# Kernel tuning notes

Measured on AMD Instinct MI355X. Metric: run time of the kernel, lower is better.

The kernel has to match this reference:

```python
import jax, jax.numpy as jnp
import numpy as np

S = 8192      # total patch tokens
NSEG = 8      # number of images/segments (equal length)
D = 1280      # embed dim
H = 16        # heads
HD = 80       # head dim
MLP = 3456    # swiglu hidden


def setup_inputs() -> dict:
    key = jax.random.key(0)
    ks = jax.random.split(key, 8)
    def w(k, shape):
        return jax.random.normal(k, shape, jnp.float32) * 0.02
    return {
        "x": jax.random.normal(ks[0], (S, 1, D), jnp.float32),
        "rotary_pos_emb": jax.random.uniform(ks[1], (S, HD // 2), jnp.float32) * 6.2831853,
        "cu_seqlens": jnp.arange(NSEG + 1, dtype=jnp.int32) * (S // NSEG),
        "norm1_w": jnp.ones((D,), jnp.float32), "norm1_b": jnp.zeros((D,), jnp.float32),
        "norm2_w": jnp.ones((D,), jnp.float32), "norm2_b": jnp.zeros((D,), jnp.float32),
        "w_qkv": w(ks[2], (3 * D, D)), "b_qkv": jnp.zeros((3 * D,), jnp.float32),
        "w_proj": w(ks[3], (D, D)), "b_proj": jnp.zeros((D,), jnp.float32),
        "w_gate": w(ks[4], (MLP, D)), "b_gate": jnp.zeros((MLP,), jnp.float32),
        "w_up": w(ks[5], (MLP, D)), "b_up": jnp.zeros((MLP,), jnp.float32),
        "w_down": w(ks[6], (D, MLP)), "b_down": jnp.zeros((D,), jnp.float32),
    }


def _ln(x, w, b, eps=1e-6):
    m = x.mean(-1, keepdims=True)
    v = ((x - m) ** 2).mean(-1, keepdims=True)
    return (x - m) * jax.lax.rsqrt(v + eps) * w + b


def _rope(x, cos, sin):
    # x: [B, S, H, HD]; cos/sin: [S, HD/2]; non-interleaved (chunk-halves) rotation
    c = jnp.concatenate([cos, cos], -1)[None, :, None, :]
    s = jnp.concatenate([sin, sin], -1)[None, :, None, :]
    x1, x2 = jnp.split(x, 2, -1)
    return x * c + jnp.concatenate([-x2, x1], -1) * s


def _forward(cu, x, freqs, norm1_w, norm1_b, norm2_w, norm2_b,
             w_qkv, b_qkv, w_proj, b_proj,
             w_gate, b_gate, w_up, b_up, w_down, b_down):
    S_, B, D_ = x.shape  # B == 1
    L = int(cu[1] - cu[0])          # equal-length segments
    nseg = len(cu) - 1
    h = _ln(x, norm1_w, norm1_b)
    qkv = h @ w_qkv.T + b_qkv                                   # [S, B, 3D]
    q, k, v = jnp.split(qkv, 3, -1)
    q, k, v = (t.reshape(S_, B, H, HD).transpose(1, 0, 2, 3) for t in (q, k, v))  # [B,S,H,d]
    cos, sin = jnp.cos(freqs), jnp.sin(freqs)
    q = _rope(q, cos, sin)
    k = _rope(k, cos, sin)
    # block-diagonal attention over cu_seqlens: fold segments into batch
    qs, ks_, vs = (t.reshape(B * nseg, L, H, HD) for t in (q, k, v))
    scale = 1.0 / np.float32(np.sqrt(HD))
    scores = jnp.einsum('blhd,bmhd->bhlm', qs, ks_) * scale     # [nseg,H,L,L]
    attn = jax.nn.softmax(scores, axis=-1)
    ctx = jnp.einsum('bhlm,bmhd->blhd', attn, vs)               # [nseg,L,H,d]
    ctx = ctx.reshape(B, S_, H * HD).transpose(1, 0, 2)         # [S,B,D]
    x = x + ctx @ w_proj.T + b_proj
    h2 = _ln(x, norm2_w, norm2_b)
    gate = jax.nn.silu(h2 @ w_gate.T + b_gate)
    up = h2 @ w_up.T + b_up
    return x + (gate * up) @ w_down.T + b_down


def reference(x, rotary_pos_emb, cu_seqlens, norm1_w, norm1_b, norm2_w, norm2_b,
              w_qkv, b_qkv, w_proj, b_proj, w_gate, b_gate, w_up, b_up,
              w_down, b_down):
    cu = np.asarray(cu_seqlens)
    return _forward(cu, x, rotary_pos_emb, norm1_w, norm1_b, norm2_w, norm2_b,
                    w_qkv, b_qkv, w_proj, b_proj,
                    w_gate, b_gate, w_up, b_up, w_down, b_down)
```

## Files before the change

### kernel.cpp

```cpp
#include <hip/hip_runtime.h>


#define S_TOK 8192
#define DIM   1280
#define NHEAD 16
#define HDIM  80
#define SEGLEN 1024
#define MLPD  3456

typedef __attribute__((ext_vector_type(8))) short bf16x8;
typedef __attribute__((ext_vector_type(8))) unsigned short u16x8;
typedef __attribute__((ext_vector_type(4))) float f32x4;

__device__ __forceinline__ float bf2f(unsigned short u) {
    unsigned int x = ((unsigned int)u) << 16;
    return __builtin_bit_cast(float, x);
}
__device__ __forceinline__ unsigned short f2bf(float f) {
    unsigned int x = __builtin_bit_cast(unsigned int, f);
    unsigned int r = x + 0x7fffu + ((x >> 16) & 1u);
    return (unsigned short)(r >> 16);
}

__device__ __forceinline__ void gload_lds16(const void* g, void* l) {
    __builtin_amdgcn_global_load_lds(
        (const __attribute__((address_space(1))) void*)g,
        (__attribute__((address_space(3))) void*)l, 16, 0, 0);
}

__device__ __forceinline__ int xcd_swz(int bid, int nwg) {
    const int q = nwg >> 3, r = nwg & 7;
    const int x = bid & 7, j = bid >> 3;
    return (x < r ? x * (q + 1) : r * (q + 1) + (x - r) * q) + j;
}

__global__ __launch_bounds__(256)
void f2b_kernel(const float* __restrict__ in, unsigned short* __restrict__ out, int n4)
{
    const int i = blockIdx.x * 256 + threadIdx.x;
    if (i >= n4) return;
    const float4 v = ((const float4*)in)[i];
    ushort4 o;
    o.x = f2bf(v.x); o.y = f2bf(v.y); o.z = f2bf(v.z); o.w = f2bf(v.w);
    ((ushort4*)out)[i] = o;
}

__global__ __launch_bounds__(256)
void ln_kernel(const float* __restrict__ xin,
               const float* __restrict__ w,
               const float* __restrict__ b,
               unsigned short* __restrict__ out)
{
    const int row = blockIdx.x;
    const int t = threadIdx.x;
    const size_t base = (size_t)row * DIM;
    float v[5];
#pragma unroll
    for (int i = 0; i < 5; ++i) v[i] = xin[base + t + i * 256];
    float s = 0.f, s2 = 0.f;
#pragma unroll
    for (int i = 0; i < 5; ++i) { s += v[i]; s2 += v[i] * v[i]; }
#pragma unroll
    for (int off = 32; off > 0; off >>= 1) {
        s  += __shfl_down(s, off);
        s2 += __shfl_down(s2, off);
    }
    __shared__ float rs[8];
    const int wave = t >> 6, lane = t & 63;
    if (lane == 0) { rs[wave] = s; rs[wave + 4] = s2; }
    __syncthreads();
    s  = rs[0] + rs[1] + rs[2] + rs[3];
    s2 = rs[4] + rs[5] + rs[6] + rs[7];
    const float mean = s * (1.f / DIM);
    const float var  = s2 * (1.f / DIM) - mean * mean;
    const float rstd = rsqrtf(var + 1e-6f);
#pragma unroll
    for (int i = 0; i < 5; ++i) {
        const int c = t + i * 256;
        out[base + c] = f2bf((v[i] - mean) * rstd * w[c] + b[c]);
    }
}

__global__ __launch_bounds__(256)
void rope_kernel(const unsigned short* __restrict__ qkv,
                 const float* __restrict__ rot,
                 unsigned short* __restrict__ qr,
                 unsigned short* __restrict__ kr)
{
    const int idx = blockIdx.x * 256 + threadIdx.x;
    const int s = idx / DIM, rem = idx % DIM;
    const int h = rem / HDIM, d = rem % HDIM;
    const int dd = (d < 40) ? d : d - 40;
    const float th = rot[s * 40 + dd];
    const float c = __cosf(th), sn = __sinf(th);
    const size_t base = (size_t)s * (3 * DIM) + h * HDIM;
    const int partner = (d < 40) ? d + 40 : d - 40;
    const float sgn = (d < 40) ? -1.f : 1.f;
    const float q  = bf2f(qkv[base + d]);
    const float k  = bf2f(qkv[DIM + base + d]);
    const float qp = bf2f(qkv[base + partner]);
    const float kp = bf2f(qkv[DIM + base + partner]);
    const float qo = q * c + sgn * qp * sn;
    const float ko = k * c + sgn * kp * sn;
    qr[idx] = f2bf(qo * 0.11180339887498949f);
    kr[idx] = f2bf(ko);
}

enum { EPI_BF16 = 0, EPI_RES = 1, EPI_GU = 2 };

template<int EPI>
__global__ __launch_bounds__(512, 2)
void gemm4q(const unsigned short* __restrict__ A,
            const unsigned short* __restrict__ B0,
            const unsigned short* __restrict__ B1,
            const float* __restrict__ bias0,
            const float* __restrict__ bias1,
            void* __restrict__ C,
            const void* __restrict__ aux,
            int M, int N, int K, int ntn)
{
    extern __shared__ __align__(16) unsigned short lds[];
    const int t = threadIdx.x;
    const int w = t >> 6, lane = t & 63;
    const int m = lane & 15, g = lane >> 4;
    const int wm = w >> 2, wn = w & 3;
    const int wg = xcd_swz(blockIdx.x, gridDim.x);
    const int nblk = wg % ntn;
    const int m0 = (wg / ntn) * 256;
    const int NT = K >> 6;

    f32x4 acc[8][4] = {};

    auto STAGE_A = [&](int tt) {
        const int k0 = tt << 6;
        unsigned short* dst = lds + (tt & 1) * 16384;
#pragma unroll
        for (int i = 0; i < 4; ++i) {
            const int ch = i * 512 + t;
            const int row = ch >> 3, c = ch & 7;
            gload_lds16(A + (size_t)(m0 + row) * K + k0 + (c ^ (row & 7)) * 8,
                        dst + ch * 8);
        }
    };
    auto STAGE_B = [&](int tt) {
        const int k0 = tt << 6;
        unsigned short* dst = lds + 32768 + (tt & 1) * 16384;
#pragma unroll
        for (int i = 0; i < 4; ++i) {
            const int ch = i * 512 + t;
            const int row = ch >> 3, c = ch & 7;
            const unsigned short* src;
            if (EPI == EPI_GU) {
                src = (row < 128)
                    ? B0 + (size_t)(nblk * 128 + row) * K
                    : B1 + (size_t)(nblk * 128 + (row - 128)) * K;
            } else {
                src = B0 + (size_t)(nblk * 256 + row) * K;
            }
            gload_lds16(src + k0 + (c ^ (row & 7)) * 8, dst + ch * 8);
        }
    };

    STAGE_A(0); STAGE_B(0);
    asm volatile("s_waitcnt vmcnt(0)" ::: "memory");
    __builtin_amdgcn_s_barrier();

    for (int tt = 0; tt < NT; ++tt) {
        const unsigned short* As = lds + (tt & 1) * 16384;
        const unsigned short* Bs = lds + 32768 + (tt & 1) * 16384;
        bf16x8 bfr[4];
#pragma unroll
        for (int kk = 0; kk < 2; ++kk) {
#pragma unroll
            for (int mh = 0; mh < 2; ++mh) {
                bf16x8 afr[4];
                const int cs = ((kk * 4 + g) ^ (m & 7)) * 8;
#pragma unroll
                for (int mf4 = 0; mf4 < 4; ++mf4) {
                    const int row = wm * 128 + (mh * 4 + mf4) * 16 + m;
                    afr[mf4] = *(const bf16x8*)&As[row * 64 + cs];
                }
                if (mh == 0) {
#pragma unroll
                    for (int nf = 0; nf < 4; ++nf) {
                        int rowb;
                        if (EPI == EPI_GU)
                            rowb = (nf < 2) ? (wn * 32 + nf * 16 + m)
                                            : (128 + wn * 32 + (nf - 2) * 16 + m);
                        else
                            rowb = wn * 64 + nf * 16 + m;
                        bfr[nf] = *(const bf16x8*)&Bs[rowb * 64 + cs];
                    }
                }
                if (kk == 0 && mh == 0 && tt + 1 < NT) STAGE_A(tt + 1);
                if (kk == 0 && mh == 1 && tt + 1 < NT) STAGE_B(tt + 1);
                if (kk == 1 && mh == 1)
                    asm volatile("s_waitcnt vmcnt(0)" ::: "memory");
                __builtin_amdgcn_s_barrier();
                __builtin_amdgcn_s_setprio(1);
#pragma unroll
                for (int mf4 = 0; mf4 < 4; ++mf4)
#pragma unroll
                    for (int nf = 0; nf < 4; ++nf)
                        acc[mh * 4 + mf4][nf] = __builtin_amdgcn_mfma_f32_16x16x32_bf16(
                            afr[mf4], bfr[nf], acc[mh * 4 + mf4][nf], 0, 0, 0);
                __builtin_amdgcn_s_setprio(0);
                __builtin_amdgcn_s_barrier();
            }
        }
    }

#pragma unroll
    for (int mf = 0; mf < 8; ++mf) {
        const int row = m0 + wm * 128 + mf * 16 + g * 4;
        if (EPI == EPI_GU) {
#pragma unroll
            for (int nfp = 0; nfp < 2; ++nfp) {
                const int col = nblk * 128 + wn * 32 + nfp * 16 + m;
                const float bgv = bias0[col], buv = bias1[col];
#pragma unroll
                for (int i = 0; i < 4; ++i) {
                    const float gv = acc[mf][nfp][i] + bgv;
                    const float uv = acc[mf][nfp + 2][i] + buv;
                    const float sg = gv / (1.f + __expf(-gv));
                    ((unsigned short*)C)[(size_t)(row + i) * N + col] = f2bf(sg * uv);
                }
            }
        } else {
#pragma unroll
            for (int nf = 0; nf < 4; ++nf) {
                const int col = nblk * 256 + wn * 64 + nf * 16 + m;
                const float bv = bias0[col];
#pragma unroll
                for (int i = 0; i < 4; ++i) {
                    const float v = acc[mf][nf][i] + bv;
                    const size_t idx = (size_t)(row + i) * N + col;
                    if (EPI == EPI_BF16) {
                        ((unsigned short*)C)[idx] = f2bf(v);
                    } else {
                        const float xr = ((const float*)aux)[idx];
                        ((float*)C)[idx] = v + xr;
                    }
                }
            }
        }
    }
}

__global__ __launch_bounds__(256)
void attn_mfma_kernel(const unsigned short* __restrict__ qr,
                      const unsigned short* __restrict__ kr,
                      const unsigned short* __restrict__ qkv,
                      unsigned short* __restrict__ ctx)
{
    const int qt = blockIdx.x, hh = blockIdx.y, seg = blockIdx.z;
    const int t = threadIdx.x;
    const int w = t >> 6, lane = t & 63;
    const int m = lane & 15, g = lane >> 4;

    __shared__ __align__(16) unsigned short Ks[64 * 80];
    __shared__ __align__(16) unsigned short Vt[80 * 72];
    __shared__ __align__(16) unsigned short Ps[4][16 * 72];

    const int q0 = seg * SEGLEN + qt * 64 + w * 16;

    bf16x8 qa0, qa1, qa2 = {};
    {
        const unsigned short* qrow = qr + (size_t)(q0 + m) * DIM + hh * HDIM;
        qa0 = *(const bf16x8*)(qrow + 8 * g);
        qa1 = *(const bf16x8*)(qrow + 32 + 8 * g);
        if (g < 2) qa2 = *(const bf16x8*)(qrow + 64 + 8 * g);
    }

    f32x4 o[5] = {};
    float mrow[4], lrow[4];
#pragma unroll
    for (int i = 0; i < 4; ++i) { mrow[i] = -1e30f; lrow[i] = 0.f; }

    for (int kt = 0; kt < SEGLEN / 64; ++kt) {
        const int kbase = seg * SEGLEN + kt * 64;
#pragma unroll
        for (int i = 0; i < 2; ++i) {
            const int ch = t + 256 * i;
            const int row = ch / 10, c = ch % 10;
            gload_lds16(kr + (size_t)(kbase + row) * DIM + hh * HDIM + c * 8,
                        &Ks[ch * 8]);
        }
        if (t < 128) {
            const int ch = 512 + t;
            const int row = ch / 10, c = ch % 10;
            gload_lds16(kr + (size_t)(kbase + row) * DIM + hh * HDIM + c * 8,
                        &Ks[ch * 8]);
        }
#pragma unroll
        for (int i = 0; i < 3; ++i) {
            const int ch = t + 256 * i;
            if (ch < 640) {
                const int k = ch & 63, dc = ch >> 6;
                const u16x8 v = *(const u16x8*)(qkv +
                    (size_t)(kbase + k) * (3 * DIM) + 2 * DIM + hh * HDIM + dc * 8);
#pragma unroll
                for (int e = 0; e < 8; ++e)
                    Vt[(dc * 8 + e) * 72 + k] = v[e];
            }
        }
        __syncthreads();

        f32x4 s[4] = {};
#pragma unroll
        for (int nn = 0; nn < 4; ++nn) {
            const unsigned short* kb = &Ks[(16 * nn + m) * 80];
            const bf16x8 b0 = *(const bf16x8*)(kb + 8 * g);
            const bf16x8 b1 = *(const bf16x8*)(kb + 32 + 8 * g);
            bf16x8 b2 = {};
            if (g < 2) b2 = *(const bf16x8*)(kb + 64 + 8 * g);
            s[nn] = __builtin_amdgcn_mfma_f32_16x16x32_bf16(qa0, b0, s[nn], 0, 0, 0);
            s[nn] = __builtin_amdgcn_mfma_f32_16x16x32_bf16(qa1, b1, s[nn], 0, 0, 0);
            s[nn] = __builtin_amdgcn_mfma_f32_16x16x32_bf16(qa2, b2, s[nn], 0, 0, 0);
        }

#pragma unroll
        for (int i = 0; i < 4; ++i) {
            float mx = fmaxf(fmaxf(s[0][i], s[1][i]), fmaxf(s[2][i], s[3][i]));
            mx = fmaxf(mx, __shfl_xor(mx, 1));
            mx = fmaxf(mx, __shfl_xor(mx, 2));
            mx = fmaxf(mx, __shfl_xor(mx, 4));
            mx = fmaxf(mx, __shfl_xor(mx, 8));
            const float mn = fmaxf(mrow[i], mx);
            const float fs = __expf(mrow[i] - mn);
            float rs = 0.f;
#pragma unroll
            for (int nn = 0; nn < 4; ++nn) {
                const float p = __expf(s[nn][i] - mn);
                s[nn][i] = p;
                rs += p;
            }
            rs += __shfl_xor(rs, 1);
            rs += __shfl_xor(rs, 2);
            rs += __shfl_xor(rs, 4);
            rs += __shfl_xor(rs, 8);
            lrow[i] = lrow[i] * fs + rs;
            mrow[i] = mn;
#pragma unroll
            for (int df = 0; df < 5; ++df) o[df][i] *= fs;
        }

#pragma unroll
        for (int nn = 0; nn < 4; ++nn)
#pragma unroll
            for (int i = 0; i < 4; ++i)
                Ps[w][(4 * g + i) * 72 + 16 * nn + m] = f2bf(s[nn][i]);

        const bf16x8 pa0 = *(const bf16x8*)&Ps[w][m * 72 + 8 * g];
        const bf16x8 pa1 = *(const bf16x8*)&Ps[w][m * 72 + 32 + 8 * g];
#pragma unroll
        for (int df = 0; df < 5; ++df) {
            const unsigned short* vb = &Vt[(16 * df + m) * 72];
            const bf16x8 vb0 = *(const bf16x8*)(vb + 8 * g);
            const bf16x8 vb1 = *(const bf16x8*)(vb + 32 + 8 * g);
            o[df] = __builtin_amdgcn_mfma_f32_16x16x32_bf16(pa0, vb0, o[df], 0, 0, 0);
            o[df] = __builtin_amdgcn_mfma_f32_16x16x32_bf16(pa1, vb1, o[df], 0, 0, 0);
        }
        __syncthreads();
    }

#pragma unroll
    for (int i = 0; i < 4; ++i) {
        const float inv = 1.f / lrow[i];
        unsigned short* crow = ctx + (size_t)(q0 + 4 * g + i) * DIM + hh * HDIM;
#pragma unroll
        for (int df = 0; df < 5; ++df)
            crow[16 * df + m] = f2bf(o[df][i] * inv);
    }
}

extern "C" void kernel_launch(void* const* d_in, const int* in_sizes, int n_in,
                              void* d_out, int out_size, void* d_ws, size_t ws_size,
                              hipStream_t stream)
{
    const float* x      = (const float*)d_in[0];
    const float* rot    = (const float*)d_in[1];
    const float* n1w    = (const float*)d_in[3];
    const float* n1b    = (const float*)d_in[4];
    const float* n2w    = (const float*)d_in[5];
    const float* n2b    = (const float*)d_in[6];
    const float* w_qkv  = (const float*)d_in[7];
    const float* b_qkv  = (const float*)d_in[8];
    const float* w_proj = (const float*)d_in[9];
    const float* b_proj = (const float*)d_in[10];
    const float* w_gate = (const float*)d_in[11];
    const float* b_gate = (const float*)d_in[12];
    const float* w_up   = (const float*)d_in[13];
    const float* b_up   = (const float*)d_in[14];
    const float* w_down = (const float*)d_in[15];
    const float* b_down = (const float*)d_in[16];

    char* ws = (char*)d_ws;
    unsigned short* qkv  = (unsigned short*)(ws + 0);
    unsigned short* h    = (unsigned short*)(ws + 62914560ull);
    unsigned short* qr   = (unsigned short*)(ws + 83886080ull);
    unsigned short* kr   = (unsigned short*)(ws + 104857600ull);
    unsigned short* ctx  = (unsigned short*)(ws + 125829120ull);
    float*          x2   = (float*)(ws + 146800640ull);
    unsigned short* wqb  = (unsigned short*)(ws + 188743680ull);
    unsigned short* wpb  = (unsigned short*)(ws + 198574080ull);
    unsigned short* wgb  = (unsigned short*)(ws + 201850880ull);
    unsigned short* wub  = (unsigned short*)(ws + 210698240ull);
    unsigned short* wdb  = (unsigned short*)(ws + 219545600ull);
    unsigned short* gbuf = qkv;

    hipFuncSetAttribute(reinterpret_cast<const void*>(gemm4q<EPI_BF16>),
                        hipFuncAttributeMaxDynamicSharedMemorySize, 131072);
    hipFuncSetAttribute(reinterpret_cast<const void*>(gemm4q<EPI_RES>),
                        hipFuncAttributeMaxDynamicSharedMemorySize, 131072);
    hipFuncSetAttribute(reinterpret_cast<const void*>(gemm4q<EPI_GU>),
                        hipFuncAttributeMaxDynamicSharedMemorySize, 131072);

    {
        const int nq = 3 * DIM * DIM / 4, np = DIM * DIM / 4, nm = MLPD * DIM / 4;
        f2b_kernel<<<(nq + 255) / 256, 256, 0, stream>>>(w_qkv,  wqb, nq);
        f2b_kernel<<<(np + 255) / 256, 256, 0, stream>>>(w_proj, wpb, np);
        f2b_kernel<<<(nm + 255) / 256, 256, 0, stream>>>(w_gate, wgb, nm);
        f2b_kernel<<<(nm + 255) / 256, 256, 0, stream>>>(w_up,   wub, nm);
        f2b_kernel<<<(nm + 255) / 256, 256, 0, stream>>>(w_down, wdb, nm);
    }

    ln_kernel<<<S_TOK, 256, 0, stream>>>(x, n1w, n1b, h);
    gemm4q<EPI_BF16><<<15 * 32, 512, 131072, stream>>>(
        h, wqb, nullptr, b_qkv, nullptr, qkv, nullptr, S_TOK, 3 * DIM, DIM, 15);
    rope_kernel<<<(S_TOK * DIM) / 256, 256, 0, stream>>>(qkv, rot, qr, kr);
    attn_mfma_kernel<<<dim3(SEGLEN / 64, NHEAD, S_TOK / SEGLEN), 256, 0, stream>>>(
        qr, kr, qkv, ctx);
    gemm4q<EPI_RES><<<5 * 32, 512, 131072, stream>>>(
        ctx, wpb, nullptr, b_proj, nullptr, x2, x, S_TOK, DIM, DIM, 5);
    ln_kernel<<<S_TOK, 256, 0, stream>>>(x2, n2w, n2b, h);
    gemm4q<EPI_GU><<<27 * 32, 512, 131072, stream>>>(
        h, wgb, wub, b_gate, b_up, gbuf, nullptr, S_TOK, MLPD, DIM, 27);
    gemm4q<EPI_RES><<<5 * 32, 512, 131072, stream>>>(
        gbuf, wdb, nullptr, b_down, nullptr, (float*)d_out, x2, S_TOK, DIM, MLPD, 5);
}
```

Measured before the change: 640.8 us.

## Split GEMM K-tile staging into halves with partial vmcnt waits

Reorganizes the GEMM's LDS layout so each 64-wide K tile is stored as two 32-wide halves, each with its own 4-way XOR swizzle. Each half is staged separately, and the loop waits with partial vmcnt counts, so compute on the first half can start while the second half is still loading. This also drops one barrier per sub-step. It aims to overlap global-to-LDS loads with MFMA work and cut synchronization stalls. The risks are more LDS bank conflicts from the narrower swizzle and fragile vmcnt accounting.

```diff
diff --git a/kernel.cpp b/kernel.cpp
--- a/kernel.cpp
+++ b/kernel.cpp
@@ -110,14 +110,14 @@
 
 template<int EPI>
 __global__ __launch_bounds__(512, 2)
-void gemm4q(const unsigned short* __restrict__ A,
-            const unsigned short* __restrict__ B0,
-            const unsigned short* __restrict__ B1,
-            const float* __restrict__ bias0,
-            const float* __restrict__ bias1,
-            void* __restrict__ C,
-            const void* __restrict__ aux,
-            int M, int N, int K, int ntn)
+void gemm_cv(const unsigned short* __restrict__ A,
+             const unsigned short* __restrict__ B0,
+             const unsigned short* __restrict__ B1,
+             const float* __restrict__ bias0,
+             const float* __restrict__ bias1,
+             void* __restrict__ C,
+             const void* __restrict__ aux,
+             int M, int N, int K, int ntn)
 {
     extern __shared__ __align__(16) unsigned short lds[];
     const int t = threadIdx.x;
@@ -131,24 +131,22 @@
 
     f32x4 acc[8][4] = {};
 
-    auto STAGE_A = [&](int tt) {
-        const int k0 = tt << 6;
-        unsigned short* dst = lds + (tt & 1) * 16384;
-#pragma unroll
-        for (int i = 0; i < 4; ++i) {
-            const int ch = i * 512 + t;
-            const int row = ch >> 3, c = ch & 7;
-            gload_lds16(A + (size_t)(m0 + row) * K + k0 + (c ^ (row & 7)) * 8,
-                        dst + ch * 8);
-        }
-    };
-    auto STAGE_B = [&](int tt) {
-        const int k0 = tt << 6;
-        unsigned short* dst = lds + 32768 + (tt & 1) * 16384;
-#pragma unroll
-        for (int i = 0; i < 4; ++i) {
-            const int ch = i * 512 + t;
-            const int row = ch >> 3, c = ch & 7;
+    auto STAGE_HALF = [&](int tt2, int h) {
+        const int k0 = tt2 << 6;
+        unsigned short* dstA = lds + (tt2 & 1) * 16384 + h * 8192;
+        unsigned short* dstB = lds + 32768 + (tt2 & 1) * 16384 + h * 8192;
+#pragma unroll
+        for (int i = 0; i < 2; ++i) {
+            const int idx = i * 512 + t;
+            const int row = idx >> 2, q = idx & 3;
+            const int G = 4 * h + (q ^ (row & 3));
+            gload_lds16(A + (size_t)(m0 + row) * K + k0 + G * 8, dstA + idx * 8);
+        }
+#pragma unroll
+        for (int i = 0; i < 2; ++i) {
+            const int idx = i * 512 + t;
+            const int row = idx >> 2, q = idx & 3;
+            const int G = 4 * h + (q ^ (row & 3));
             const unsigned short* src;
             if (EPI == EPI_GU) {
                 src = (row < 128)
@@ -157,30 +155,41 @@
             } else {
                 src = B0 + (size_t)(nblk * 256 + row) * K;
             }
-            gload_lds16(src + k0 + (c ^ (row & 7)) * 8, dst + ch * 8);
+            gload_lds16(src + k0 + G * 8, dstB + idx * 8);
         }
     };
 
-    STAGE_A(0); STAGE_B(0);
-    asm volatile("s_waitcnt vmcnt(0)" ::: "memory");
-    __builtin_amdgcn_s_barrier();
+    STAGE_HALF(0, 0);
+    STAGE_HALF(0, 1);
+
+    const int qs = (g ^ (m & 3)) * 8;
 
     for (int tt = 0; tt < NT; ++tt) {
         const unsigned short* As = lds + (tt & 1) * 16384;
         const unsigned short* Bs = lds + 32768 + (tt & 1) * 16384;
+        const bool pf = (tt + 1 < NT);
         bf16x8 bfr[4];
 #pragma unroll
         for (int kk = 0; kk < 2; ++kk) {
 #pragma unroll
             for (int mh = 0; mh < 2; ++mh) {
+                if (kk == 0 && mh == 0)
+                    asm volatile("s_waitcnt vmcnt(4)" ::: "memory");
+                if (kk == 1 && mh == 0) {
+                    if (pf) asm volatile("s_waitcnt vmcnt(8)" ::: "memory");
+                    else    asm volatile("s_waitcnt vmcnt(0)" ::: "memory");
+                }
+                __builtin_amdgcn_s_barrier();
+                __builtin_amdgcn_sched_barrier(0);
+                const unsigned short* Ah = As + kk * 8192;
                 bf16x8 afr[4];
-                const int cs = ((kk * 4 + g) ^ (m & 7)) * 8;
 #pragma unroll
                 for (int mf4 = 0; mf4 < 4; ++mf4) {
                     const int row = wm * 128 + (mh * 4 + mf4) * 16 + m;
-                    afr[mf4] = *(const bf16x8*)&As[row * 64 + cs];
+                    afr[mf4] = *(const bf16x8*)&Ah[row * 32 + qs];
                 }
                 if (mh == 0) {
+                    const unsigned short* Bh = Bs + kk * 8192;
 #pragma unroll
                     for (int nf = 0; nf < 4; ++nf) {
                         int rowb;
@@ -189,14 +198,11 @@
                                             : (128 + wn * 32 + (nf - 2) * 16 + m);
                         else
                             rowb = wn * 64 + nf * 16 + m;
-                        bfr[nf] = *(const bf16x8*)&Bs[rowb * 64 + cs];
+                        bfr[nf] = *(const bf16x8*)&Bh[rowb * 32 + qs];
                     }
                 }
-                if (kk == 0 && mh == 0 && tt + 1 < NT) STAGE_A(tt + 1);
-                if (kk == 0 && mh == 1 && tt + 1 < NT) STAGE_B(tt + 1);
-                if (kk == 1 && mh == 1)
-                    asm volatile("s_waitcnt vmcnt(0)" ::: "memory");
-                __builtin_amdgcn_s_barrier();
+                if (pf && kk == 0 && mh == 0) STAGE_HALF(tt + 1, 0);
+                if (pf && kk == 0 && mh == 1) STAGE_HALF(tt + 1, 1);
                 __builtin_amdgcn_s_setprio(1);
 #pragma unroll
                 for (int mf4 = 0; mf4 < 4; ++mf4)
@@ -205,7 +211,6 @@
                         acc[mh * 4 + mf4][nf] = __builtin_amdgcn_mfma_f32_16x16x32_bf16(
                             afr[mf4], bfr[nf], acc[mh * 4 + mf4][nf], 0, 0, 0);
                 __builtin_amdgcn_s_setprio(0);
-                __builtin_amdgcn_s_barrier();
             }
         }
     }
@@ -409,11 +414,11 @@
     unsigned short* wdb  = (unsigned short*)(ws + 219545600ull);
     unsigned short* gbuf = qkv;
 
-    hipFuncSetAttribute(reinterpret_cast<const void*>(gemm4q<EPI_BF16>),
+    hipFuncSetAttribute(reinterpret_cast<const void*>(gemm_cv<EPI_BF16>),
                         hipFuncAttributeMaxDynamicSharedMemorySize, 131072);
-    hipFuncSetAttribute(reinterpret_cast<const void*>(gemm4q<EPI_RES>),
+    hipFuncSetAttribute(reinterpret_cast<const void*>(gemm_cv<EPI_RES>),
                         hipFuncAttributeMaxDynamicSharedMemorySize, 131072);
-    hipFuncSetAttribute(reinterpret_cast<const void*>(gemm4q<EPI_GU>),
+    hipFuncSetAttribute(reinterpret_cast<const void*>(gemm_cv<EPI_GU>),
                         hipFuncAttributeMaxDynamicSharedMemorySize, 131072);
 
     {
@@ -426,16 +431,16 @@
     }
 
     ln_kernel<<<S_TOK, 256, 0, stream>>>(x, n1w, n1b, h);
-    gemm4q<EPI_BF16><<<15 * 32, 512, 131072, stream>>>(
+    gemm_cv<EPI_BF16><<<15 * 32, 512, 131072, stream>>>(
         h, wqb, nullptr, b_qkv, nullptr, qkv, nullptr, S_TOK, 3 * DIM, DIM, 15);
     rope_kernel<<<(S_TOK * DIM) / 256, 256, 0, stream>>>(qkv, rot, qr, kr);
     attn_mfma_kernel<<<dim3(SEGLEN / 64, NHEAD, S_TOK / SEGLEN), 256, 0, stream>>>(
         qr, kr, qkv, ctx);
-    gemm4q<EPI_RES><<<5 * 32, 512, 131072, stream>>>(
+    gemm_cv<EPI_RES><<<5 * 32, 512, 131072, stream>>>(
         ctx, wpb, nullptr, b_proj, nullptr, x2, x, S_TOK, DIM, DIM, 5);
     ln_kernel<<<S_TOK, 256, 0, stream>>>(x2, n2w, n2b, h);
-    gemm4q<EPI_GU><<<27 * 32, 512, 131072, stream>>>(
+    gemm_cv<EPI_GU><<<27 * 32, 512, 131072, stream>>>(
         h, wgb, wub, b_gate, b_up, gbuf, nullptr, S_TOK, MLPD, DIM, 27);
-    gemm4q<EPI_RES><<<5 * 32, 512, 131072, stream>>>(
+    gemm_cv<EPI_RES><<<5 * 32, 512, 131072, stream>>>(
         gbuf, wdb, nullptr, b_down, nullptr, (float*)d_out, x2, S_TOK, DIM, MLPD, 5);
 }
```

Result: slower. 695.0 us (+8.5%).
